# Kernel optimization log

Measured on AMD Instinct MI355X. Metric: run time of the kernel, lower is better.

The kernel has to match this reference:

```python
import math
import jax, jax.numpy as jnp
import numpy as np

EPS = 1e-5
NUM_HEADER = 2


def pos_encoding(C, T, dtype):
    i = jnp.arange(C)
    exp = -((i - (i % 2)).astype(dtype) / C)
    freqs = jnp.power(jnp.asarray(10000.0, dtype), exp)[:, None]      # [C,1]
    phases = ((i % 2).astype(dtype) * (np.pi / 2))[:, None]           # [C,1]
    pos = jnp.arange(T, dtype=dtype)[None, :]                         # [1,T]
    return jnp.sin(pos * freqs + phases)                              # [C,T]


def layernorm2d(x, g, b):
    # LayerNorm over (C,T) jointly, per batch element (nn.LayerNorm([C, length]))
    mu = jnp.mean(x, axis=(1, 2), keepdims=True)
    var = jnp.mean((x - mu) ** 2, axis=(1, 2), keepdims=True)
    return (x - mu) * jax.lax.rsqrt(var + EPS) * g[None] + b[None]


def dsconv(x, dw_w, dw_b, pw_w, pw_b):
    # depthwise conv1d (groups=C, 'same' padding for odd k) + pointwise 1x1
    C = x.shape[1]
    k = dw_w.shape[-1]
    y = jax.lax.conv_general_dilated(
        x, dw_w[:, None, :], (1,), [(k // 2, k // 2)],
        dimension_numbers=('NCH', 'OIH', 'NCH'), feature_group_count=C)
    y = y + dw_b[None, :, None]
    y = jnp.einsum('bct,oc->bot', y, pw_w) + pw_b[None, :, None]
    return y


def attention(x, mask, Wq, Wk, Wv, Wo):
    # Faithful to source bug: all heads use Wqs[1]/Wks[1]/Wvs[1] -> identical heads.
    xt = jnp.transpose(x, (0, 2, 1))          # [B,T,C]
    C = xt.shape[-1]
    dk = C / NUM_HEADER
    q = xt @ Wq                               # [B,T,dk]
    k_ = xt @ Wk
    v = xt @ Wv
    s = jnp.einsum('bqd,bkd->bqk', q, k_) * (1.0 / math.sqrt(dk))
    hmask = mask[:, None, :]                  # mask over keys
    s = s * hmask + (1 - hmask) * (-1e30)
    a = jax.nn.softmax(s, axis=2) * mask[:, :, None]
    head = a @ v                              # [B,T,dk]
    heads = jnp.tile(head, (1, 1, NUM_HEADER))  # concat of identical heads
    out = heads @ Wo                          # [B,T,C]
    return jnp.transpose(out, (0, 2, 1))      # [B,C,T]


def setup_inputs() -> dict:
    key = jax.random.key(0)
    B, C, T = 16, 128, 1024
    NCONV, K = 4, 7
    dk = C // NUM_HEADER
    ks = jax.random.split(key, 12)
    inp = {
        'x': jax.random.normal(ks[0], (B, C, T), jnp.float32),
        'mask': jnp.ones((B, T), jnp.float32),
        'dw_w': jax.random.normal(ks[1], (NCONV, C, K), jnp.float32) * math.sqrt(2.0 / K),
        'dw_b': jnp.zeros((NCONV, C), jnp.float32),
        'pw_w': jax.random.normal(ks[2], (NCONV, C, C), jnp.float32) * math.sqrt(2.0 / C),
        'pw_b': jnp.zeros((NCONV, C), jnp.float32),
        'norm0_g': jnp.ones((C, T), jnp.float32),
        'norm0_b': jnp.zeros((C, T), jnp.float32),
        'norms_g': jnp.ones((NCONV, C, T), jnp.float32),
        'norms_b': jnp.zeros((NCONV, C, T), jnp.float32),
        'norme_g': jnp.ones((C, T), jnp.float32),
        'norme_b': jnp.zeros((C, T), jnp.float32),
        'Wq': jax.random.normal(ks[3], (C, dk), jnp.float32) * math.sqrt(2.0 / (C + dk)),
        'Wk': jax.random.normal(ks[4], (C, dk), jnp.float32) * math.sqrt(2.0 / (C + dk)),
        'Wv': jax.random.normal(ks[5], (C, dk), jnp.float32) * math.sqrt(2.0 / (C + dk)),
        'Wo': jax.random.normal(ks[6], (C, C), jnp.float32) * math.sqrt(2.0 / C),
        'fc_w': jax.random.normal(ks[7], (C, C), jnp.float32) * (0.1 * math.sqrt(6.0 / (2 * C))),
        'fc_b': jnp.zeros((C,), jnp.float32),
    }
    return inp


def reference(x, mask, dw_w, dw_b, pw_w, pw_b, norm0_g, norm0_b,
              norms_g, norms_b, norme_g, norme_b,
              Wq, Wk, Wv, Wo, fc_w, fc_b):
    B, C, T = x.shape
    nconv = dw_w.shape[0]
    # dropout is identity in eval mode (reference is deterministic)
    out = x + pos_encoding(C, T, x.dtype)[None]
    res = layernorm2d(out, norm0_g, norm0_b)
    for i in range(nconv):
        out = dsconv(out, dw_w[i], dw_b[i], pw_w[i], pw_b[i])
        out = jax.nn.relu(out)
        out = out + res
        res = out
        out = layernorm2d(out, norms_g[i], norms_b[i])
    out = attention(out, mask, Wq, Wk, Wv, Wo)
    out = out + res
    res = out
    out = layernorm2d(out, norme_g, norme_b)
    out = jnp.einsum('bct,oc->bot', out, fc_w) + fc_b[None, :, None]
    out = jax.nn.relu(out)
    out = out + res
    return out
```

## Files before the change

kernel.cpp:

```cpp
#include <hip/hip_runtime.h>
#include <math.h>

#define BB 16
#define CC 128
#define TT 1024
#define KK 7
#define DK 64
#define NSPLIT 4

typedef float f32x4 __attribute__((ext_vector_type(4)));
typedef short s16x8 __attribute__((ext_vector_type(8)));

__device__ inline short f2bf(float f) {
  union { float f; unsigned u; } v; v.f = f;
  unsigned r = (v.u + 0x7FFFu + ((v.u >> 16) & 1u)) >> 16;
  return (short)r;
}

__device__ inline void block_partial_256(float s, float ss, float* dst) {
#pragma unroll
  for (int off = 32; off; off >>= 1) { s += __shfl_xor(s, off); ss += __shfl_xor(ss, off); }
  __shared__ float red[8];
  int w = threadIdx.x >> 6;
  if ((threadIdx.x & 63) == 0) { red[2 * w] = s; red[2 * w + 1] = ss; }
  __syncthreads();
  if (threadIdx.x == 0) {
    for (int i = 1; i < 4; ++i) { s += red[2 * i]; ss += red[2 * i + 1]; }
    dst[0] = s; dst[1] = ss;
  }
}

__device__ inline void ln_stats_from_parts(const float* part_batch, int n, float* sh) {
  if (threadIdx.x < 64) {
    float s = 0.f, ss = 0.f;
    for (int i = threadIdx.x; i < n; i += 64) { s += part_batch[2 * i]; ss += part_batch[2 * i + 1]; }
#pragma unroll
    for (int off = 32; off; off >>= 1) { s += __shfl_xor(s, off); ss += __shfl_xor(ss, off); }
    if (threadIdx.x == 0) {
      const float invN = 1.f / (float)(CC * TT);
      float mu = s * invN;
      sh[0] = mu;
      sh[1] = rsqrtf(ss * invN - mu * mu + 1e-5f);
    }
  }
  __syncthreads();
}

__global__ __launch_bounds__(256) void k_prep(const float* __restrict__ pww,
                                              const float* __restrict__ Wq,
                                              const float* __restrict__ Wk,
                                              const float* __restrict__ Wv,
                                              const float* __restrict__ Wo,
                                              const float* __restrict__ fcw,
                                              short* __restrict__ pwwb,
                                              short* __restrict__ wqkvb,
                                              short* __restrict__ wo2b,
                                              short* __restrict__ fcwb) {
  int i = blockIdx.x * 256 + threadIdx.x;
  if (i < 65536) { pwwb[i] = f2bf(pww[i]); return; }
  i -= 65536;
  if (i < 24576) {
    int m = i >> 7, c = i & 127;
    int sel = m >> 6, d = m & 63;
    const float* srcp = sel == 0 ? Wq : (sel == 1 ? Wk : Wv);
    wqkvb[i] = f2bf(srcp[c * DK + d]);
    return;
  }
  i -= 24576;
  if (i < 8192) {
    int o = i >> 6, d = i & 63;
    wo2b[i] = f2bf(Wo[d * CC + o] + Wo[(d + 64) * CC + o]);
    return;
  }
  i -= 8192;
  fcwb[i] = f2bf(fcw[i]);
}

__global__ __launch_bounds__(256) void k_addpos(const float* __restrict__ x,
                                                float* __restrict__ out,
                                                float* __restrict__ part) {
  int bc = blockIdx.x;
  int c = bc & (CC - 1);
  float ce = (float)(c & ~1);
  float freq = expf(-(ce / (float)CC) * 9.210340371976184f);
  float phase = (c & 1) ? 1.5707963267948966f : 0.0f;
  const float* xr = x + (size_t)bc * TT;
  float* orow = out + (size_t)bc * TT;
  float s = 0.f, ss = 0.f;
  for (int t = threadIdx.x; t < TT; t += 256) {
    float v = xr[t] + sinf((float)t * freq + phase);
    orow[t] = v;
    s += v; ss += v * v;
  }
  block_partial_256(s, ss, part + (size_t)bc * 2);
}

template <bool LN_IN, bool LN_RES>
__global__ __launch_bounds__(256) void k_dsconv(const float* __restrict__ in,
                                                const float* __restrict__ lng,
                                                const float* __restrict__ lnb,
                                                const float* __restrict__ part_in, int npart,
                                                const float* __restrict__ dww,
                                                const float* __restrict__ dwb,
                                                const short* __restrict__ pwwb,
                                                const float* __restrict__ pwb,
                                                float* __restrict__ out,
                                                float* __restrict__ part_out) {
  int tile = blockIdx.x & 31, b = blockIdx.x >> 5;
  int t0 = tile * 32;
  __shared__ float stats[2];
  __shared__ float xs[CC][39];
  __shared__ __align__(16) short Dt[32][136];
  ln_stats_from_parts(part_in + (size_t)b * npart * 2, npart, stats);
  float mu = stats[0], rs = stats[1];

  for (int i = threadIdx.x; i < CC * 38; i += 256) {
    int c = i / 38, j = i - c * 38;
    int t = t0 + j - 3;
    float v = 0.f;
    if (t >= 0 && t < TT) {
      v = in[((size_t)b * CC + c) * TT + t];
      if (LN_IN) v = (v - mu) * rs * lng[c * TT + t] + lnb[c * TT + t];
    }
    xs[c][j] = v;
  }
  __syncthreads();
  for (int i = threadIdx.x; i < 32 * CC; i += 256) {
    int t = i >> 7, c = i & 127;
    float a = dwb[c];
#pragma unroll
    for (int j = 0; j < KK; ++j) a += dww[c * KK + j] * xs[c][t + j];
    Dt[t][c] = f2bf(a);
  }
  __syncthreads();

  int w = threadIdx.x >> 6, lane = threadIdx.x & 63;
  int lo = lane & 15, hi = lane >> 4;
  f32x4 acc[2][2];
#pragma unroll
  for (int mt = 0; mt < 2; ++mt)
#pragma unroll
    for (int nt = 0; nt < 2; ++nt) { acc[mt][nt][0] = 0.f; acc[mt][nt][1] = 0.f; acc[mt][nt][2] = 0.f; acc[mt][nt][3] = 0.f; }
#pragma unroll
  for (int ks = 0; ks < 4; ++ks) {
    s16x8 b0 = *(const s16x8*)&Dt[lo][ks * 32 + hi * 8];
    s16x8 b1 = *(const s16x8*)&Dt[16 + lo][ks * 32 + hi * 8];
    s16x8 a0 = *(const s16x8*)&pwwb[(size_t)(w * 32 + lo) * CC + ks * 32 + hi * 8];
    s16x8 a1 = *(const s16x8*)&pwwb[(size_t)(w * 32 + 16 + lo) * CC + ks * 32 + hi * 8];
    acc[0][0] = __builtin_amdgcn_mfma_f32_16x16x32_bf16(a0, b0, acc[0][0], 0, 0, 0);
    acc[0][1] = __builtin_amdgcn_mfma_f32_16x16x32_bf16(a0, b1, acc[0][1], 0, 0, 0);
    acc[1][0] = __builtin_amdgcn_mfma_f32_16x16x32_bf16(a1, b0, acc[1][0], 0, 0, 0);
    acc[1][1] = __builtin_amdgcn_mfma_f32_16x16x32_bf16(a1, b1, acc[1][1], 0, 0, 0);
  }

  float s = 0.f, ss = 0.f;
#pragma unroll
  for (int mt = 0; mt < 2; ++mt)
#pragma unroll
    for (int nt = 0; nt < 2; ++nt)
#pragma unroll
      for (int r = 0; r < 4; ++r) {
        int row = w * 32 + mt * 16 + hi * 4 + r;
        int t = t0 + nt * 16 + lo;
        float v = acc[mt][nt][r] + pwb[row];
        v = v > 0.f ? v : 0.f;
        size_t idx = ((size_t)b * CC + row) * TT + t;
        float rv = in[idx];
        if (LN_RES) rv = (rv - mu) * rs * lng[row * TT + t] + lnb[row * TT + t];
        v += rv;
        out[idx] = v;
        s += v; ss += v * v;
      }
  block_partial_256(s, ss, part_out + (size_t)blockIdx.x * 2);
}

__global__ __launch_bounds__(256) void k_qkv(const float* __restrict__ in,
                                             const float* __restrict__ lng,
                                             const float* __restrict__ lnb,
                                             const float* __restrict__ part_in,
                                             const short* __restrict__ wqkvb,
                                             short* __restrict__ q,
                                             short* __restrict__ k,
                                             short* __restrict__ vt) {
  int tile = blockIdx.x & 31, b = blockIdx.x >> 5;
  int t0 = tile * 32;
  __shared__ float stats[2];
  __shared__ __align__(16) short Dt[32][136];
  ln_stats_from_parts(part_in + (size_t)b * 64, 32, stats);
  float mu = stats[0], rs = stats[1];
  for (int i = threadIdx.x; i < CC * 32; i += 256) {
    int c = i >> 5, t = i & 31;
    float v = in[((size_t)b * CC + c) * TT + t0 + t];
    Dt[t][c] = f2bf((v - mu) * rs * lng[c * TT + t0 + t] + lnb[c * TT + t0 + t]);
  }
  __syncthreads();

  int w = threadIdx.x >> 6, lane = threadIdx.x & 63;
  int lo = lane & 15, hi = lane >> 4;
  f32x4 acc[3][2];
#pragma unroll
  for (int mt = 0; mt < 3; ++mt)
#pragma unroll
    for (int nt = 0; nt < 2; ++nt) { acc[mt][nt][0] = 0.f; acc[mt][nt][1] = 0.f; acc[mt][nt][2] = 0.f; acc[mt][nt][3] = 0.f; }
#pragma unroll
  for (int ks = 0; ks < 4; ++ks) {
    s16x8 b0 = *(const s16x8*)&Dt[lo][ks * 32 + hi * 8];
    s16x8 b1 = *(const s16x8*)&Dt[16 + lo][ks * 32 + hi * 8];
#pragma unroll
    for (int mt = 0; mt < 3; ++mt) {
      s16x8 a = *(const s16x8*)&wqkvb[(size_t)(w * 48 + mt * 16 + lo) * CC + ks * 32 + hi * 8];
      acc[mt][0] = __builtin_amdgcn_mfma_f32_16x16x32_bf16(a, b0, acc[mt][0], 0, 0, 0);
      acc[mt][1] = __builtin_amdgcn_mfma_f32_16x16x32_bf16(a, b1, acc[mt][1], 0, 0, 0);
    }
  }
#pragma unroll
  for (int mt = 0; mt < 3; ++mt)
#pragma unroll
    for (int nt = 0; nt < 2; ++nt) {
      int m0 = w * 48 + mt * 16 + hi * 4;
      int t = t0 + nt * 16 + lo;
      short4 pk;
      pk.x = f2bf(acc[mt][nt][0]); pk.y = f2bf(acc[mt][nt][1]);
      pk.z = f2bf(acc[mt][nt][2]); pk.w = f2bf(acc[mt][nt][3]);
      if (m0 < 64) {
        *(short4*)(q + ((size_t)b * TT + t) * DK + m0) = pk;
      } else if (m0 < 128) {
        *(short4*)(k + ((size_t)b * TT + t) * DK + (m0 - 64)) = pk;
      } else {
        int d = m0 - 128;
        vt[((size_t)b * DK + d) * TT + t] = pk.x;
        vt[((size_t)b * DK + d + 1) * TT + t] = pk.y;
        vt[((size_t)b * DK + d + 2) * TT + t] = pk.z;
        vt[((size_t)b * DK + d + 3) * TT + t] = pk.w;
      }
    }
}

__global__ __launch_bounds__(128) void k_attn(const short* __restrict__ qb,
                                              const short* __restrict__ kbuf,
                                              const short* __restrict__ vtb,
                                              const float* __restrict__ mask,
                                              float* __restrict__ pacc,
                                              float* __restrict__ pml) {
  int sp = blockIdx.x & (NSPLIT - 1);
  int qt = (blockIdx.x >> 2) & 31;
  int b = blockIdx.x >> 7;
  int w = threadIdx.x >> 6, lane = threadIdx.x & 63;
  int lo = lane & 15, hi = lane >> 4;

  __shared__ __align__(16) short ks[64][72];
  __shared__ __align__(16) short vt[64][72];
  __shared__ __align__(16) short ps[2][16][68];
  __shared__ float ms[64];

  const short* qp = qb + ((size_t)b * TT + qt * 32 + w * 16 + lo) * DK + hi * 8;
  s16x8 aq0 = *(const s16x8*)qp;
  s16x8 aq1 = *(const s16x8*)(qp + 32);

  f32x4 acc[4];
  float m_i[4], l_i[4];
#pragma unroll
  for (int r = 0; r < 4; ++r) {
    m_i[r] = -3.0e38f; l_i[r] = 0.f;
#pragma unroll
    for (int nt = 0; nt < 4; ++nt) acc[nt][r] = 0.f;
  }
  const float scale = 0.125f;

  for (int kb2 = sp * (TT / 64 / NSPLIT); kb2 < (sp + 1) * (TT / 64 / NSPLIT); ++kb2) {
    __syncthreads();
    for (int i = threadIdx.x; i < 512; i += 128) {
      int r = i >> 3, ch = i & 7;
      *(s16x8*)&ks[r][ch * 8] =
          *(const s16x8*)(kbuf + ((size_t)b * TT + kb2 * 64 + r) * DK + ch * 8);
      *(s16x8*)&vt[r][ch * 8] =
          *(const s16x8*)(vtb + ((size_t)b * DK + r) * TT + kb2 * 64 + ch * 8);
    }
    if (threadIdx.x < 64) ms[threadIdx.x] = mask[(size_t)b * TT + kb2 * 64 + threadIdx.x];
    __syncthreads();

    f32x4 sc[4];
#pragma unroll
    for (int nt = 0; nt < 4; ++nt) {
      f32x4 z; z[0] = 0.f; z[1] = 0.f; z[2] = 0.f; z[3] = 0.f;
      s16x8 bk0 = *(const s16x8*)&ks[nt * 16 + lo][hi * 8];
      s16x8 bk1 = *(const s16x8*)&ks[nt * 16 + lo][32 + hi * 8];
      z = __builtin_amdgcn_mfma_f32_16x16x32_bf16(aq0, bk0, z, 0, 0, 0);
      z = __builtin_amdgcn_mfma_f32_16x16x32_bf16(aq1, bk1, z, 0, 0, 0);
      sc[nt] = z;
    }
#pragma unroll
    for (int nt = 0; nt < 4; ++nt) {
      float mv = ms[nt * 16 + lo];
      float addv = (1.f - mv) * -1e30f;
#pragma unroll
      for (int r = 0; r < 4; ++r) sc[nt][r] = sc[nt][r] * scale * mv + addv;
    }
    float alpha[4];
#pragma unroll
    for (int r = 0; r < 4; ++r) {
      float m0 = fmaxf(fmaxf(sc[0][r], sc[1][r]), fmaxf(sc[2][r], sc[3][r]));
#pragma unroll
      for (int off = 1; off < 16; off <<= 1) m0 = fmaxf(m0, __shfl_xor(m0, off));
      float mn = fmaxf(m_i[r], m0);
      alpha[r] = __expf(m_i[r] - mn);
      m_i[r] = mn;
    }
    float psum[4] = {0.f, 0.f, 0.f, 0.f};
#pragma unroll
    for (int nt = 0; nt < 4; ++nt)
#pragma unroll
      for (int r = 0; r < 4; ++r) {
        float p = __expf(sc[nt][r] - m_i[r]);
        psum[r] += p;
        ps[w][hi * 4 + r][nt * 16 + lo] = f2bf(p);
      }
#pragma unroll
    for (int r = 0; r < 4; ++r) {
      float sum = psum[r];
#pragma unroll
      for (int off = 1; off < 16; off <<= 1) sum += __shfl_xor(sum, off);
      l_i[r] = l_i[r] * alpha[r] + sum;
    }
#pragma unroll
    for (int nt = 0; nt < 4; ++nt)
#pragma unroll
      for (int r = 0; r < 4; ++r) acc[nt][r] *= alpha[r];

    s16x8 ap0 = *(const s16x8*)&ps[w][lo][hi * 8];
    s16x8 ap1 = *(const s16x8*)&ps[w][lo][32 + hi * 8];
#pragma unroll
    for (int nt = 0; nt < 4; ++nt) {
      s16x8 bv0 = *(const s16x8*)&vt[nt * 16 + lo][hi * 8];
      s16x8 bv1 = *(const s16x8*)&vt[nt * 16 + lo][32 + hi * 8];
      acc[nt] = __builtin_amdgcn_mfma_f32_16x16x32_bf16(ap0, bv0, acc[nt], 0, 0, 0);
      acc[nt] = __builtin_amdgcn_mfma_f32_16x16x32_bf16(ap1, bv1, acc[nt], 0, 0, 0);
    }
  }
#pragma unroll
  for (int r = 0; r < 4; ++r) {
    int row = qt * 32 + w * 16 + hi * 4 + r;
    size_t pb = (((size_t)b * TT + row) * NSPLIT + sp) * DK;
#pragma unroll
    for (int nt = 0; nt < 4; ++nt) pacc[pb + nt * 16 + lo] = acc[nt][r];
    if (lo == 0) {
      size_t mb = (((size_t)b * TT + row) * NSPLIT + sp) * 2;
      pml[mb] = m_i[r];
      pml[mb + 1] = l_i[r];
    }
  }
}

__global__ __launch_bounds__(256) void k_attn_combine(const float* __restrict__ pacc,
                                                      const float* __restrict__ pml,
                                                      const float* __restrict__ mask,
                                                      short* __restrict__ head) {
  int tid = blockIdx.x * 256 + threadIdx.x;
  int chunk = tid & 3;
  int row = (tid >> 2) & (TT - 1);
  int b = tid >> 12;
  size_t rb = (size_t)b * TT + row;
  float m[NSPLIT], l[NSPLIT];
#pragma unroll
  for (int s = 0; s < NSPLIT; ++s) {
    m[s] = pml[(rb * NSPLIT + s) * 2];
    l[s] = pml[(rb * NSPLIT + s) * 2 + 1];
  }
  float M = fmaxf(fmaxf(m[0], m[1]), fmaxf(m[2], m[3]));
  float wgt[NSPLIT], L = 0.f;
#pragma unroll
  for (int s = 0; s < NSPLIT; ++s) { wgt[s] = __expf(m[s] - M); L += wgt[s] * l[s]; }
  float inv = mask[rb] / L;
  float o[16];
#pragma unroll
  for (int j = 0; j < 16; ++j) o[j] = 0.f;
#pragma unroll
  for (int s = 0; s < NSPLIT; ++s) {
    const float4* pa = (const float4*)(pacc + (rb * NSPLIT + s) * DK + chunk * 16);
#pragma unroll
    for (int j4 = 0; j4 < 4; ++j4) {
      float4 v = pa[j4];
      o[j4 * 4] += wgt[s] * v.x; o[j4 * 4 + 1] += wgt[s] * v.y;
      o[j4 * 4 + 2] += wgt[s] * v.z; o[j4 * 4 + 3] += wgt[s] * v.w;
    }
  }
  short h[16];
#pragma unroll
  for (int j = 0; j < 16; ++j) h[j] = f2bf(o[j] * inv);
  *(uint4*)(head + rb * DK + chunk * 16) = *(uint4*)h;
  *(uint4*)(head + rb * DK + chunk * 16 + 8) = *(uint4*)(h + 8);
}

__global__ __launch_bounds__(256) void k_attnout(const short* __restrict__ head,
                                                 const short* __restrict__ wo2b,
                                                 const float* __restrict__ res,
                                                 float* __restrict__ out,
                                                 float* __restrict__ part_out) {
  int tile = blockIdx.x & 31, b = blockIdx.x >> 5;
  int t0 = tile * 32;
  __shared__ __align__(16) short Ht[32][72];
  {
    int i = threadIdx.x;
    int t = i >> 3, ch = i & 7;
    *(s16x8*)&Ht[t][ch * 8] =
        *(const s16x8*)(head + ((size_t)b * TT + t0 + t) * DK + ch * 8);
  }
  __syncthreads();

  int w = threadIdx.x >> 6, lane = threadIdx.x & 63;
  int lo = lane & 15, hi = lane >> 4;
  f32x4 acc[2][2];
#pragma unroll
  for (int mt = 0; mt < 2; ++mt)
#pragma unroll
    for (int nt = 0; nt < 2; ++nt) { acc[mt][nt][0] = 0.f; acc[mt][nt][1] = 0.f; acc[mt][nt][2] = 0.f; acc[mt][nt][3] = 0.f; }
#pragma unroll
  for (int ks = 0; ks < 2; ++ks) {
    s16x8 b0 = *(const s16x8*)&Ht[lo][ks * 32 + hi * 8];
    s16x8 b1 = *(const s16x8*)&Ht[16 + lo][ks * 32 + hi * 8];
    s16x8 a0 = *(const s16x8*)&wo2b[(size_t)(w * 32 + lo) * DK + ks * 32 + hi * 8];
    s16x8 a1 = *(const s16x8*)&wo2b[(size_t)(w * 32 + 16 + lo) * DK + ks * 32 + hi * 8];
    acc[0][0] = __builtin_amdgcn_mfma_f32_16x16x32_bf16(a0, b0, acc[0][0], 0, 0, 0);
    acc[0][1] = __builtin_amdgcn_mfma_f32_16x16x32_bf16(a0, b1, acc[0][1], 0, 0, 0);
    acc[1][0] = __builtin_amdgcn_mfma_f32_16x16x32_bf16(a1, b0, acc[1][0], 0, 0, 0);
    acc[1][1] = __builtin_amdgcn_mfma_f32_16x16x32_bf16(a1, b1, acc[1][1], 0, 0, 0);
  }
  float s = 0.f, ss = 0.f;
#pragma unroll
  for (int mt = 0; mt < 2; ++mt)
#pragma unroll
    for (int nt = 0; nt < 2; ++nt)
#pragma unroll
      for (int r = 0; r < 4; ++r) {
        int row = w * 32 + mt * 16 + hi * 4 + r;
        int t = t0 + nt * 16 + lo;
        size_t idx = ((size_t)b * CC + row) * TT + t;
        float v = acc[mt][nt][r] + res[idx];
        out[idx] = v;
        s += v; ss += v * v;
      }
  block_partial_256(s, ss, part_out + (size_t)blockIdx.x * 2);
}

__global__ __launch_bounds__(256) void k_fc(const float* __restrict__ in,
                                            const float* __restrict__ lng,
                                            const float* __restrict__ lnb,
                                            const float* __restrict__ part_in,
                                            const short* __restrict__ fcwb,
                                            const float* __restrict__ fb,
                                            float* __restrict__ out) {
  int tile = blockIdx.x & 31, b = blockIdx.x >> 5;
  int t0 = tile * 32;
  __shared__ float stats[2];
  __shared__ __align__(16) short Dt[32][136];
  ln_stats_from_parts(part_in + (size_t)b * 64, 32, stats);
  float mu = stats[0], rs = stats[1];
  for (int i = threadIdx.x; i < CC * 32; i += 256) {
    int c = i >> 5, t = i & 31;
    float v = in[((size_t)b * CC + c) * TT + t0 + t];
    Dt[t][c] = f2bf((v - mu) * rs * lng[c * TT + t0 + t] + lnb[c * TT + t0 + t]);
  }
  __syncthreads();

  int w = threadIdx.x >> 6, lane = threadIdx.x & 63;
  int lo = lane & 15, hi = lane >> 4;
  f32x4 acc[2][2];
#pragma unroll
  for (int mt = 0; mt < 2; ++mt)
#pragma unroll
    for (int nt = 0; nt < 2; ++nt) { acc[mt][nt][0] = 0.f; acc[mt][nt][1] = 0.f; acc[mt][nt][2] = 0.f; acc[mt][nt][3] = 0.f; }
#pragma unroll
  for (int ks = 0; ks < 4; ++ks) {
    s16x8 b0 = *(const s16x8*)&Dt[lo][ks * 32 + hi * 8];
    s16x8 b1 = *(const s16x8*)&Dt[16 + lo][ks * 32 + hi * 8];
    s16x8 a0 = *(const s16x8*)&fcwb[(size_t)(w * 32 + lo) * CC + ks * 32 + hi * 8];
    s16x8 a1 = *(const s16x8*)&fcwb[(size_t)(w * 32 + 16 + lo) * CC + ks * 32 + hi * 8];
    acc[0][0] = __builtin_amdgcn_mfma_f32_16x16x32_bf16(a0, b0, acc[0][0], 0, 0, 0);
    acc[0][1] = __builtin_amdgcn_mfma_f32_16x16x32_bf16(a0, b1, acc[0][1], 0, 0, 0);
    acc[1][0] = __builtin_amdgcn_mfma_f32_16x16x32_bf16(a1, b0, acc[1][0], 0, 0, 0);
    acc[1][1] = __builtin_amdgcn_mfma_f32_16x16x32_bf16(a1, b1, acc[1][1], 0, 0, 0);
  }
#pragma unroll
  for (int mt = 0; mt < 2; ++mt)
#pragma unroll
    for (int nt = 0; nt < 2; ++nt)
#pragma unroll
      for (int r = 0; r < 4; ++r) {
        int row = w * 32 + mt * 16 + hi * 4 + r;
        int t = t0 + nt * 16 + lo;
        size_t idx = ((size_t)b * CC + row) * TT + t;
        float v = acc[mt][nt][r] + fb[row];
        v = v > 0.f ? v : 0.f;
        out[idx] = v + in[idx];
      }
}

extern "C" void kernel_launch(void* const* d_in, const int* in_sizes, int n_in,
                              void* d_out, int out_size, void* d_ws, size_t ws_size,
                              hipStream_t stream) {
  const float* x    = (const float*)d_in[0];
  const float* mask = (const float*)d_in[1];
  const float* dww  = (const float*)d_in[2];
  const float* dwb  = (const float*)d_in[3];
  const float* pww  = (const float*)d_in[4];
  const float* pwb  = (const float*)d_in[5];
  const float* n0g  = (const float*)d_in[6];
  const float* n0b  = (const float*)d_in[7];
  const float* nsg  = (const float*)d_in[8];
  const float* nsb  = (const float*)d_in[9];
  const float* neg_ = (const float*)d_in[10];
  const float* neb  = (const float*)d_in[11];
  const float* Wq   = (const float*)d_in[12];
  const float* Wk   = (const float*)d_in[13];
  const float* Wv   = (const float*)d_in[14];
  const float* Wo   = (const float*)d_in[15];
  const float* fcw  = (const float*)d_in[16];
  const float* fcb  = (const float*)d_in[17];
  float* out = (float*)d_out;

  float* W = (float*)d_ws;
  const size_t NBCT = (size_t)BB * CC * TT;
  const size_t NBTD = (size_t)BB * TT * DK;
  const size_t CT = (size_t)CC * TT;
  float* O     = W;
  float* S     = W + NBCT;
  float* PART0 = W + 2 * NBCT;
  float* PARTS = PART0 + 4096;
  float* PACC  = PARTS + 5 * 1024;
  float* PML   = PACC + NBTD * NSPLIT;
  short* QB    = (short*)(PML + (size_t)BB * TT * NSPLIT * 2);
  short* KB    = QB + NBTD;
  short* VT    = KB + NBTD;
  short* HDB   = VT + NBTD;
  short* PWWB  = HDB + NBTD;
  short* WQKVB = PWWB + 65536;
  short* WO2B  = WQKVB + 24576;
  short* FCWB  = WO2B + 8192;

  k_prep<<<448, 256, 0, stream>>>(pww, Wq, Wk, Wv, Wo, fcw, PWWB, WQKVB, WO2B, FCWB);
  k_addpos<<<BB * CC, 256, 0, stream>>>(x, O, PART0);
  k_dsconv<false, true><<<BB * 32, 256, 0, stream>>>(
      O, n0g, n0b, PART0, 128, dww, dwb, PWWB, pwb, S, PARTS);
  k_dsconv<true, false><<<BB * 32, 256, 0, stream>>>(
      S, nsg + 0 * CT, nsb + 0 * CT, PARTS, 32,
      dww + 1 * CC * KK, dwb + 1 * CC, PWWB + 1 * CC * CC, pwb + 1 * CC, O, PARTS + 1024);
  k_dsconv<true, false><<<BB * 32, 256, 0, stream>>>(
      O, nsg + 1 * CT, nsb + 1 * CT, PARTS + 1024, 32,
      dww + 2 * CC * KK, dwb + 2 * CC, PWWB + 2 * CC * CC, pwb + 2 * CC, S, PARTS + 2048);
  k_dsconv<true, false><<<BB * 32, 256, 0, stream>>>(
      S, nsg + 2 * CT, nsb + 2 * CT, PARTS + 2048, 32,
      dww + 3 * CC * KK, dwb + 3 * CC, PWWB + 3 * CC * CC, pwb + 3 * CC, O, PARTS + 3072);
  k_qkv<<<BB * 32, 256, 0, stream>>>(O, nsg + 3 * CT, nsb + 3 * CT, PARTS + 3072,
                                     WQKVB, QB, KB, VT);
  k_attn<<<BB * 32 * NSPLIT, 128, 0, stream>>>(QB, KB, VT, mask, PACC, PML);
  k_attn_combine<<<BB * TT * 4 / 256, 256, 0, stream>>>(PACC, PML, mask, HDB);
  k_attnout<<<BB * 32, 256, 0, stream>>>(HDB, WO2B, O, S, PARTS + 4096);
  k_fc<<<BB * 32, 256, 0, stream>>>(S, neg_, neb, PARTS + 4096, FCWB, fcb, out);
}
```

Measured before the change: 218.9 us.

## Vectorize loads, reuse staged tiles for residuals, fuse attention combine, bf16 partials

Several changes land together. The add-pos, dsconv, qkv and fc kernels now use float4 global loads, and the dsconv and fc kernels take the residual from the shared-memory tile they already staged instead of reading global memory again. The split-attention partial accumulators are stored as bf16 instead of fp32, and the combine step is folded into the attention-output projection kernel, which removes one launch and one intermediate buffer. In exchange, the bf16 partials lose precision before the split-K combine, and the extra shared-memory arrays raise LDS use per block.

```diff
diff --git a/kernel.cpp b/kernel.cpp
--- a/kernel.cpp
+++ b/kernel.cpp
@@ -15,6 +15,12 @@
   union { float f; unsigned u; } v; v.f = f;
   unsigned r = (v.u + 0x7FFFu + ((v.u >> 16) & 1u)) >> 16;
   return (short)r;
+}
+
+__device__ inline float bf2f(short s) {
+  union { unsigned u; float f; } v;
+  v.u = ((unsigned)(unsigned short)s) << 16;
+  return v.f;
 }
 
 __device__ inline void block_partial_256(float s, float ss, float* dst) {
@@ -86,12 +92,15 @@
   float phase = (c & 1) ? 1.5707963267948966f : 0.0f;
   const float* xr = x + (size_t)bc * TT;
   float* orow = out + (size_t)bc * TT;
-  float s = 0.f, ss = 0.f;
-  for (int t = threadIdx.x; t < TT; t += 256) {
-    float v = xr[t] + sinf((float)t * freq + phase);
-    orow[t] = v;
-    s += v; ss += v * v;
-  }
+  int t = threadIdx.x * 4;
+  float4 v = *(const float4*)(xr + t);
+  v.x += sinf((float)(t + 0) * freq + phase);
+  v.y += sinf((float)(t + 1) * freq + phase);
+  v.z += sinf((float)(t + 2) * freq + phase);
+  v.w += sinf((float)(t + 3) * freq + phase);
+  *(float4*)(orow + t) = v;
+  float s = v.x + v.y + v.z + v.w;
+  float ss = v.x * v.x + v.y * v.y + v.z * v.z + v.w * v.w;
   block_partial_256(s, ss, part + (size_t)bc * 2);
 }
 
@@ -109,27 +118,59 @@
   int tile = blockIdx.x & 31, b = blockIdx.x >> 5;
   int t0 = tile * 32;
   __shared__ float stats[2];
-  __shared__ float xs[CC][39];
+  __shared__ float xs[CC][41];
+  __shared__ float xr2[LN_IN ? CC : 1][33];
   __shared__ __align__(16) short Dt[32][136];
   ln_stats_from_parts(part_in + (size_t)b * npart * 2, npart, stats);
   float mu = stats[0], rs = stats[1];
 
-  for (int i = threadIdx.x; i < CC * 38; i += 256) {
-    int c = i / 38, j = i - c * 38;
-    int t = t0 + j - 3;
-    float v = 0.f;
-    if (t >= 0 && t < TT) {
-      v = in[((size_t)b * CC + c) * TT + t];
-      if (LN_IN) v = (v - mu) * rs * lng[c * TT + t] + lnb[c * TT + t];
-    }
-    xs[c][j] = v;
+  for (int i = threadIdx.x; i < CC * 10; i += 256) {
+    int c = i / 10, q = i - c * 10;
+    int tb = t0 - 4 + q * 4;
+    const float* rowp = in + ((size_t)b * CC + c) * TT;
+    float r0, r1, r2, r3, o0, o1, o2, o3;
+    bool full = (tb >= 0) && (tb + 4 <= TT);
+    if (full) {
+      float4 v = *(const float4*)(rowp + tb);
+      r0 = v.x; r1 = v.y; r2 = v.z; r3 = v.w;
+      o0 = r0; o1 = r1; o2 = r2; o3 = r3;
+      if (LN_IN) {
+        float4 g = *(const float4*)(lng + (size_t)c * TT + tb);
+        float4 bv = *(const float4*)(lnb + (size_t)c * TT + tb);
+        o0 = (r0 - mu) * rs * g.x + bv.x;
+        o1 = (r1 - mu) * rs * g.y + bv.y;
+        o2 = (r2 - mu) * rs * g.z + bv.z;
+        o3 = (r3 - mu) * rs * g.w + bv.w;
+      }
+    } else {
+      float rr[4], oo[4];
+#pragma unroll
+      for (int k = 0; k < 4; ++k) {
+        int t = tb + k;
+        bool inb = (t >= 0) && (t < TT);
+        float rv = inb ? rowp[t] : 0.f;
+        rr[k] = rv;
+        float ov = rv;
+        if (LN_IN && inb)
+          ov = (rv - mu) * rs * lng[(size_t)c * TT + t] + lnb[(size_t)c * TT + t];
+        oo[k] = ov;
+      }
+      r0 = rr[0]; r1 = rr[1]; r2 = rr[2]; r3 = rr[3];
+      o0 = oo[0]; o1 = oo[1]; o2 = oo[2]; o3 = oo[3];
+    }
+    if (LN_IN && q >= 1 && q <= 8) {
+      int tl = (q - 1) * 4;
+      xr2[c][tl] = r0; xr2[c][tl + 1] = r1; xr2[c][tl + 2] = r2; xr2[c][tl + 3] = r3;
+    }
+    int base = q * 4;
+    xs[c][base] = o0; xs[c][base + 1] = o1; xs[c][base + 2] = o2; xs[c][base + 3] = o3;
   }
   __syncthreads();
   for (int i = threadIdx.x; i < 32 * CC; i += 256) {
     int t = i >> 7, c = i & 127;
     float a = dwb[c];
 #pragma unroll
-    for (int j = 0; j < KK; ++j) a += dww[c * KK + j] * xs[c][t + j];
+    for (int j = 0; j < KK; ++j) a += dww[c * KK + j] * xs[c][t + j + 1];
     Dt[t][c] = f2bf(a);
   }
   __syncthreads();
@@ -161,14 +202,21 @@
 #pragma unroll
       for (int r = 0; r < 4; ++r) {
         int row = w * 32 + mt * 16 + hi * 4 + r;
-        int t = t0 + nt * 16 + lo;
+        int tl = nt * 16 + lo;
+        int t = t0 + tl;
         float v = acc[mt][nt][r] + pwb[row];
         v = v > 0.f ? v : 0.f;
-        size_t idx = ((size_t)b * CC + row) * TT + t;
-        float rv = in[idx];
-        if (LN_RES) rv = (rv - mu) * rs * lng[row * TT + t] + lnb[row * TT + t];
+        float rv;
+        if (LN_RES) {
+          float raw = xs[row][tl + 4];
+          rv = (raw - mu) * rs * lng[row * TT + t] + lnb[row * TT + t];
+        } else if (LN_IN) {
+          rv = xr2[row][tl];
+        } else {
+          rv = xs[row][tl + 4];
+        }
         v += rv;
-        out[idx] = v;
+        out[((size_t)b * CC + row) * TT + t] = v;
         s += v; ss += v * v;
       }
   block_partial_256(s, ss, part_out + (size_t)blockIdx.x * 2);
@@ -188,10 +236,17 @@
   __shared__ __align__(16) short Dt[32][136];
   ln_stats_from_parts(part_in + (size_t)b * 64, 32, stats);
   float mu = stats[0], rs = stats[1];
-  for (int i = threadIdx.x; i < CC * 32; i += 256) {
-    int c = i >> 5, t = i & 31;
-    float v = in[((size_t)b * CC + c) * TT + t0 + t];
-    Dt[t][c] = f2bf((v - mu) * rs * lng[c * TT + t0 + t] + lnb[c * TT + t0 + t]);
+  for (int i = threadIdx.x; i < CC * 8; i += 256) {
+    int c = i >> 3, qq = i & 7;
+    int t = qq * 4;
+    size_t off = (size_t)c * TT + t0 + t;
+    float4 v = *(const float4*)(in + (size_t)b * CC * TT + off);
+    float4 g = *(const float4*)(lng + off);
+    float4 bb = *(const float4*)(lnb + off);
+    Dt[t + 0][c] = f2bf((v.x - mu) * rs * g.x + bb.x);
+    Dt[t + 1][c] = f2bf((v.y - mu) * rs * g.y + bb.y);
+    Dt[t + 2][c] = f2bf((v.z - mu) * rs * g.z + bb.z);
+    Dt[t + 3][c] = f2bf((v.w - mu) * rs * g.w + bb.w);
   }
   __syncthreads();
 
@@ -240,7 +295,7 @@
                                               const short* __restrict__ kbuf,
                                               const short* __restrict__ vtb,
                                               const float* __restrict__ mask,
-                                              float* __restrict__ pacc,
+                                              short* __restrict__ pacch,
                                               float* __restrict__ pml) {
   int sp = blockIdx.x & (NSPLIT - 1);
   int qt = (blockIdx.x >> 2) & 31;
@@ -342,7 +397,7 @@
     int row = qt * 32 + w * 16 + hi * 4 + r;
     size_t pb = (((size_t)b * TT + row) * NSPLIT + sp) * DK;
 #pragma unroll
-    for (int nt = 0; nt < 4; ++nt) pacc[pb + nt * 16 + lo] = acc[nt][r];
+    for (int nt = 0; nt < 4; ++nt) pacch[pb + nt * 16 + lo] = f2bf(acc[nt][r]);
     if (lo == 0) {
       size_t mb = (((size_t)b * TT + row) * NSPLIT + sp) * 2;
       pml[mb] = m_i[r];
@@ -351,59 +406,42 @@
   }
 }
 
-__global__ __launch_bounds__(256) void k_attn_combine(const float* __restrict__ pacc,
-                                                      const float* __restrict__ pml,
-                                                      const float* __restrict__ mask,
-                                                      short* __restrict__ head) {
-  int tid = blockIdx.x * 256 + threadIdx.x;
-  int chunk = tid & 3;
-  int row = (tid >> 2) & (TT - 1);
-  int b = tid >> 12;
-  size_t rb = (size_t)b * TT + row;
-  float m[NSPLIT], l[NSPLIT];
-#pragma unroll
-  for (int s = 0; s < NSPLIT; ++s) {
-    m[s] = pml[(rb * NSPLIT + s) * 2];
-    l[s] = pml[(rb * NSPLIT + s) * 2 + 1];
-  }
-  float M = fmaxf(fmaxf(m[0], m[1]), fmaxf(m[2], m[3]));
-  float wgt[NSPLIT], L = 0.f;
-#pragma unroll
-  for (int s = 0; s < NSPLIT; ++s) { wgt[s] = __expf(m[s] - M); L += wgt[s] * l[s]; }
-  float inv = mask[rb] / L;
-  float o[16];
-#pragma unroll
-  for (int j = 0; j < 16; ++j) o[j] = 0.f;
-#pragma unroll
-  for (int s = 0; s < NSPLIT; ++s) {
-    const float4* pa = (const float4*)(pacc + (rb * NSPLIT + s) * DK + chunk * 16);
-#pragma unroll
-    for (int j4 = 0; j4 < 4; ++j4) {
-      float4 v = pa[j4];
-      o[j4 * 4] += wgt[s] * v.x; o[j4 * 4 + 1] += wgt[s] * v.y;
-      o[j4 * 4 + 2] += wgt[s] * v.z; o[j4 * 4 + 3] += wgt[s] * v.w;
-    }
-  }
-  short h[16];
-#pragma unroll
-  for (int j = 0; j < 16; ++j) h[j] = f2bf(o[j] * inv);
-  *(uint4*)(head + rb * DK + chunk * 16) = *(uint4*)h;
-  *(uint4*)(head + rb * DK + chunk * 16 + 8) = *(uint4*)(h + 8);
-}
-
-__global__ __launch_bounds__(256) void k_attnout(const short* __restrict__ head,
-                                                 const short* __restrict__ wo2b,
-                                                 const float* __restrict__ res,
-                                                 float* __restrict__ out,
-                                                 float* __restrict__ part_out) {
+__global__ __launch_bounds__(256) void k_attnout2(const short* __restrict__ pacch,
+                                                  const float* __restrict__ pml,
+                                                  const float* __restrict__ mask,
+                                                  const short* __restrict__ wo2b,
+                                                  const float* __restrict__ res,
+                                                  float* __restrict__ out,
+                                                  float* __restrict__ part_out) {
   int tile = blockIdx.x & 31, b = blockIdx.x >> 5;
   int t0 = tile * 32;
   __shared__ __align__(16) short Ht[32][72];
   {
     int i = threadIdx.x;
-    int t = i >> 3, ch = i & 7;
-    *(s16x8*)&Ht[t][ch * 8] =
-        *(const s16x8*)(head + ((size_t)b * TT + t0 + t) * DK + ch * 8);
+    int tr = i >> 3, q = i & 7;
+    size_t rb = (size_t)b * TT + t0 + tr;
+    float m[NSPLIT], l[NSPLIT];
+#pragma unroll
+    for (int s = 0; s < NSPLIT; ++s) {
+      m[s] = pml[(rb * NSPLIT + s) * 2];
+      l[s] = pml[(rb * NSPLIT + s) * 2 + 1];
+    }
+    float M = fmaxf(fmaxf(m[0], m[1]), fmaxf(m[2], m[3]));
+    float wgt[NSPLIT], L = 0.f;
+#pragma unroll
+    for (int s = 0; s < NSPLIT; ++s) { wgt[s] = __expf(m[s] - M); L += wgt[s] * l[s]; }
+    float inv = mask[rb] / L;
+    float o[8] = {0.f, 0.f, 0.f, 0.f, 0.f, 0.f, 0.f, 0.f};
+#pragma unroll
+    for (int s = 0; s < NSPLIT; ++s) {
+      s16x8 pv = *(const s16x8*)(pacch + (rb * NSPLIT + s) * DK + q * 8);
+#pragma unroll
+      for (int j = 0; j < 8; ++j) o[j] += wgt[s] * bf2f(pv[j]);
+    }
+    short h[8];
+#pragma unroll
+    for (int j = 0; j < 8; ++j) h[j] = f2bf(o[j] * inv);
+    *(s16x8*)&Ht[tr][q * 8] = *(const s16x8*)h;
   }
   __syncthreads();
 
@@ -452,13 +490,22 @@
   int tile = blockIdx.x & 31, b = blockIdx.x >> 5;
   int t0 = tile * 32;
   __shared__ float stats[2];
+  __shared__ float xr2[CC][33];
   __shared__ __align__(16) short Dt[32][136];
   ln_stats_from_parts(part_in + (size_t)b * 64, 32, stats);
   float mu = stats[0], rs = stats[1];
-  for (int i = threadIdx.x; i < CC * 32; i += 256) {
-    int c = i >> 5, t = i & 31;
-    float v = in[((size_t)b * CC + c) * TT + t0 + t];
-    Dt[t][c] = f2bf((v - mu) * rs * lng[c * TT + t0 + t] + lnb[c * TT + t0 + t]);
+  for (int i = threadIdx.x; i < CC * 8; i += 256) {
+    int c = i >> 3, q = i & 7;
+    int t = q * 4;
+    size_t off = (size_t)c * TT + t0 + t;
+    float4 v = *(const float4*)(in + (size_t)b * CC * TT + off);
+    float4 g = *(const float4*)(lng + off);
+    float4 bb = *(const float4*)(lnb + off);
+    xr2[c][t] = v.x; xr2[c][t + 1] = v.y; xr2[c][t + 2] = v.z; xr2[c][t + 3] = v.w;
+    Dt[t + 0][c] = f2bf((v.x - mu) * rs * g.x + bb.x);
+    Dt[t + 1][c] = f2bf((v.y - mu) * rs * g.y + bb.y);
+    Dt[t + 2][c] = f2bf((v.z - mu) * rs * g.z + bb.z);
+    Dt[t + 3][c] = f2bf((v.w - mu) * rs * g.w + bb.w);
   }
   __syncthreads();
 
@@ -487,11 +534,12 @@
 #pragma unroll
       for (int r = 0; r < 4; ++r) {
         int row = w * 32 + mt * 16 + hi * 4 + r;
-        int t = t0 + nt * 16 + lo;
+        int tl = nt * 16 + lo;
+        int t = t0 + tl;
         size_t idx = ((size_t)b * CC + row) * TT + t;
         float v = acc[mt][nt][r] + fb[row];
         v = v > 0.f ? v : 0.f;
-        out[idx] = v + in[idx];
+        out[idx] = v + xr2[row][tl];
       }
 }
 
@@ -526,13 +574,12 @@
   float* S     = W + NBCT;
   float* PART0 = W + 2 * NBCT;
   float* PARTS = PART0 + 4096;
-  float* PACC  = PARTS + 5 * 1024;
-  float* PML   = PACC + NBTD * NSPLIT;
+  float* PML   = PARTS + 5 * 1024;
   short* QB    = (short*)(PML + (size_t)BB * TT * NSPLIT * 2);
   short* KB    = QB + NBTD;
   short* VT    = KB + NBTD;
-  short* HDB   = VT + NBTD;
-  short* PWWB  = HDB + NBTD;
+  short* PACCH = VT + NBTD;
+  short* PWWB  = PACCH + NBTD * NSPLIT;
   short* WQKVB = PWWB + 65536;
   short* WO2B  = WQKVB + 24576;
   short* FCWB  = WO2B + 8192;
@@ -552,8 +599,7 @@
       dww + 3 * CC * KK, dwb + 3 * CC, PWWB + 3 * CC * CC, pwb + 3 * CC, O, PARTS + 3072);
   k_qkv<<<BB * 32, 256, 0, stream>>>(O, nsg + 3 * CT, nsb + 3 * CT, PARTS + 3072,
                                      WQKVB, QB, KB, VT);
-  k_attn<<<BB * 32 * NSPLIT, 128, 0, stream>>>(QB, KB, VT, mask, PACC, PML);
-  k_attn_combine<<<BB * TT * 4 / 256, 256, 0, stream>>>(PACC, PML, mask, HDB);
-  k_attnout<<<BB * 32, 256, 0, stream>>>(HDB, WO2B, O, S, PARTS + 4096);
+  k_attn<<<BB * 32 * NSPLIT, 128, 0, stream>>>(QB, KB, VT, mask, PACCH, PML);
+  k_attnout2<<<BB * 32, 256, 0, stream>>>(PACCH, PML, mask, WO2B, O, S, PARTS + 4096);
   k_fc<<<BB * 32, 256, 0, stream>>>(S, neg_, neb, PARTS + 4096, FCWB, fcb, out);
 }
```

Measured after the change: 194.2 us. -11.3%, faster.
